# Kernel tuning notes

Measured on AMD Instinct MI355X. Metric: run time of the kernel, lower is better.

## Reference

```python
import math
import jax, jax.numpy as jnp
import numpy as np

N, C, H, W, G = 32, 128, 56, 56, 32
SHIFT = 1  # fixed value for random.randint(-1, 1) chosen at module init


def _unfold_h(x):
    # F.unfold(x, (3,1), dilation=(2,1), padding=(2,0)) -> (n, c, 3, h, w)
    p = jnp.pad(x, ((0, 0), (0, 0), (2, 2), (0, 0)))
    return jnp.stack([p[:, :, 0:H], p[:, :, 2:H + 2], p[:, :, 4:H + 4]], axis=2)


def _unfold_w(x):
    # F.unfold(x, (1,3), dilation=(1,2), padding=(0,2)) -> (n, c, 3, h, w)
    p = jnp.pad(x, ((0, 0), (0, 0), (0, 0), (2, 2)))
    return jnp.stack([p[:, :, :, 0:W], p[:, :, :, 2:W + 2], p[:, :, :, 4:W + 4]], axis=2)


def setup_inputs() -> dict:
    key = jax.random.key(0)
    k1, k2, k3, k4 = jax.random.split(key, 4)
    x = jax.random.normal(k1, (N, C, H, W), dtype=jnp.float32)
    p2w = jax.random.normal(k2, (1, C, 3, H, W), dtype=jnp.float32) * 0.02
    p5w = jax.random.normal(k3, (1, C, 1, 1), dtype=jnp.float32) * 0.02
    conv_w = jax.random.normal(k4, (C // G, C), dtype=jnp.float32) * 0.02  # 1x1 conv, no bias
    return {"x": x, "p2w": p2w, "p5w": p5w, "conv_w": conv_w}


def reference(x, p2w, p5w, conv_w):
    n = x.shape[0]
    t1 = _unfold_h(x)                      # (n, c, 3, h, w)
    t2 = p2w * t1                          # (n, c, 3, h, w)
    t3 = _unfold_w(x)                      # (n, c, 3, h, w)
    t4 = jnp.roll(x, SHIFT, axis=2)        # roll along height
    t5 = p5w * t4
    t6 = t4 + x
    t2f = t2.reshape(n, C * 3, H * W)
    t6f = t6.reshape(n, C, H * W)
    # bmm: (n, c*3, hw) x (n, hw, c) -> (n, c*3, c)
    t7 = jnp.einsum('nkp,ncp->nkc', t2f, t6f) / math.sqrt(H * W)
    # 1x1 conv: (c//g, c) applied pointwise
    t8 = jnp.einsum('oc,nchw->nohw', conv_w, t5)            # (n, c//g, h, w)
    t9 = (t8[:, None] * x.reshape(n, G, C // G, H, W)).reshape(n, C, H, W)
    t3f = t3.reshape(n, C * 3, H * W)
    # bmm: (n, c, c*3) x (n, c*3, hw) -> (n, c, hw)
    t10 = (jnp.einsum('nkc,nkp->ncp', t7, t3f) / math.sqrt(C * 3)).reshape(n, C, H, W)
    return t9 + t10
```

## Files before the change

### kernel.cpp

```cpp
#include <hip/hip_runtime.h>

#define NB 32
#define CCH 128
#define HH 56
#define WWD 56
#define HWP (HH*WWD)
#define K3C (3*CCH)
#define SPLITK 8

typedef _Float16 half8 __attribute__((ext_vector_type(8)));
typedef float floatx4 __attribute__((ext_vector_type(4)));

__global__ __launch_bounds__(256) void cvtp2w_kernel(const float* __restrict__ src,
                                                     _Float16* __restrict__ dst) {
    const int row = blockIdx.x;
    const int j = row >> 7;
    const int c = row & 127;
    const float* s = src + ((size_t)c * 3 + j) * HWP;
    _Float16* d = dst + (size_t)row * HWP;
    for (int base = threadIdx.x * 8; base < HWP; base += 2048) {
        const float4 a = *(const float4*)(s + base);
        const float4 b = *(const float4*)(s + base + 4);
        half8 v;
        v[0] = (_Float16)a.x; v[1] = (_Float16)a.y; v[2] = (_Float16)a.z; v[3] = (_Float16)a.w;
        v[4] = (_Float16)b.x; v[5] = (_Float16)b.y; v[6] = (_Float16)b.z; v[7] = (_Float16)b.w;
        *(half8*)(d + base) = v;
    }
}

__global__ __launch_bounds__(256) void cvt_xt_kernel(const float* __restrict__ x,
                                                     _Float16* __restrict__ xh,
                                                     _Float16* __restrict__ xT) {
    __shared__ _Float16 t[64 * 72];
    const int bid = blockIdx.x;
    const int r8  = bid & 7;
    const int g   = bid >> 3;
    const int n   = r8 + 8 * (g / 98);
    const int rem = g % 98;
    const int c0  = (rem / 49) * 64;
    const int p0  = (rem % 49) * 64;
    const int tid = threadIdx.x;
    const int r   = tid >> 2;
    const int seg = (tid & 3) * 16;

    const float* src = x + ((size_t)n * CCH + c0 + r) * HWP + p0 + seg;
    const float4 a0 = *(const float4*)(src);
    const float4 a1 = *(const float4*)(src + 4);
    const float4 a2 = *(const float4*)(src + 8);
    const float4 a3 = *(const float4*)(src + 12);
    half8 v0, v1;
    v0[0] = (_Float16)a0.x; v0[1] = (_Float16)a0.y; v0[2] = (_Float16)a0.z; v0[3] = (_Float16)a0.w;
    v0[4] = (_Float16)a1.x; v0[5] = (_Float16)a1.y; v0[6] = (_Float16)a1.z; v0[7] = (_Float16)a1.w;
    v1[0] = (_Float16)a2.x; v1[1] = (_Float16)a2.y; v1[2] = (_Float16)a2.z; v1[3] = (_Float16)a2.w;
    v1[4] = (_Float16)a3.x; v1[5] = (_Float16)a3.y; v1[6] = (_Float16)a3.z; v1[7] = (_Float16)a3.w;

    _Float16* dxh = xh + ((size_t)n * CCH + c0 + r) * HWP + p0 + seg;
    *(half8*)(dxh)     = v0;
    *(half8*)(dxh + 8) = v1;
    *(half8*)(&t[r * 72 + seg])     = v0;
    *(half8*)(&t[r * 72 + seg + 8]) = v1;
    __syncthreads();
    _Float16* dst = xT + ((size_t)n * HWP + p0 + r) * CCH + c0 + seg;
    half8 w0, w1;
#pragma unroll
    for (int i = 0; i < 8; ++i) w0[i] = t[(seg + i) * 72 + r];
#pragma unroll
    for (int i = 0; i < 8; ++i) w1[i] = t[(seg + 8 + i) * 72 + r];
    *(half8*)(dst) = w0;
    *(half8*)(dst + 8) = w1;
}

__global__ __launch_bounds__(64) void t8_kernel(const _Float16* __restrict__ xh,
                                                const float* __restrict__ conv_w,
                                                const float* __restrict__ p5w,
                                                float* __restrict__ t8) {
    const int bid = blockIdx.x;
    const int r8  = bid & 7;
    const int g   = bid >> 3;
    const int n   = r8 + 8 * (g / 49);
    const int p   = (g % 49) * 64 + threadIdx.x;
    const int proll = (p >= WWD) ? (p - WWD) : (p + (HH - 1) * WWD);
    const _Float16* xb = xh + (size_t)n * CCH * HWP + proll;
    float a0 = 0.f, a1 = 0.f, a2 = 0.f, a3 = 0.f;
#pragma unroll 4
    for (int c = 0; c < CCH; ++c) {
        const float xp = (float)xb[(size_t)c * HWP] * p5w[c];
        a0 += conv_w[c] * xp;
        a1 += conv_w[CCH + c] * xp;
        a2 += conv_w[2 * CCH + c] * xp;
        a3 += conv_w[3 * CCH + c] * xp;
    }
    float* dst = t8 + (size_t)n * 4 * HWP + p;
    dst[0] = a0; dst[HWP] = a1; dst[2 * HWP] = a2; dst[3 * HWP] = a3;
}

__global__ __launch_bounds__(256) void gemm1_kernel(const _Float16* __restrict__ xh,
                                                    const _Float16* __restrict__ p2wh,
                                                    _Float16* __restrict__ part) {
    __shared__ _Float16 As[128 * 72];
    __shared__ _Float16 Bs[128 * 72];

    const int bid   = blockIdx.x;
    const int r8    = bid & 7;
    const int g     = bid >> 3;
    const int n     = r8 + 8 * (g / 24);
    const int inner = g % 24;
    const int jb    = inner % 3;
    const int m0    = jb * 128;
    const int s     = inner / 3;
    const int i0    = (s * 49) >> 3;
    const int i1    = ((s + 1) * 49) >> 3;

    const int tid = threadIdx.x;
    const int r   = tid >> 1;
    const int c0  = (tid & 1) * 32;

    const int ashift = 112 * (jb - 1);
    const _Float16* xa = xh + ((size_t)n * CCH + r) * HWP;
    const _Float16* pw = p2wh + (size_t)(m0 + r) * HWP;

    const int wave = tid >> 6;
    const int lane = tid & 63;
    const int l15  = lane & 15;
    const int quad = lane >> 4;
    const int wm   = (wave >> 1) * 64;
    const int wn   = (wave & 1) * 64;

    floatx4 acc[4][4];
#pragma unroll
    for (int a = 0; a < 4; ++a)
#pragma unroll
        for (int b = 0; b < 4; ++b) acc[a][b] = (floatx4){0.f,0.f,0.f,0.f};

    half8 xv[4], wv[4], uv[4], vv[4];

    {
        const int p0 = i0 * 64;
#pragma unroll
        for (int seg = 0; seg < 4; ++seg) {
            const int col  = c0 + seg * 8;
            const int pA   = p0 + col;
            const int srcp = pA + ashift;
            if (srcp >= 0 && srcp < HWP) {
                xv[seg] = *(const half8*)(xa + srcp);
                wv[seg] = *(const half8*)(pw + pA);
            } else {
#pragma unroll
                for (int i = 0; i < 8; ++i) { xv[seg][i] = (_Float16)0.f; wv[seg][i] = (_Float16)0.f; }
            }
            const int proll = (pA >= WWD) ? (pA - WWD) : (pA + (HH - 1) * WWD);
            uv[seg] = *(const half8*)(xa + pA);
            vv[seg] = *(const half8*)(xa + proll);
        }
    }

    for (int it = i0; it < i1; ++it) {
#pragma unroll
        for (int seg = 0; seg < 4; ++seg) {
            const int col = c0 + seg * 8;
            *(half8*)(&As[r * 72 + col]) = xv[seg] * wv[seg];
            *(half8*)(&Bs[r * 72 + col]) = uv[seg] + vv[seg];
        }
        __syncthreads();
        if (it + 1 < i1) {
            const int p0 = (it + 1) * 64;
#pragma unroll
            for (int seg = 0; seg < 4; ++seg) {
                const int col  = c0 + seg * 8;
                const int pA   = p0 + col;
                const int srcp = pA + ashift;
                if (srcp >= 0 && srcp < HWP) {
                    xv[seg] = *(const half8*)(xa + srcp);
                    wv[seg] = *(const half8*)(pw + pA);
                } else {
#pragma unroll
                    for (int i = 0; i < 8; ++i) { xv[seg][i] = (_Float16)0.f; wv[seg][i] = (_Float16)0.f; }
                }
                const int proll = (pA >= WWD) ? (pA - WWD) : (pA + (HH - 1) * WWD);
                uv[seg] = *(const half8*)(xa + pA);
                vv[seg] = *(const half8*)(xa + proll);
            }
        }
#pragma unroll
        for (int ks = 0; ks < 2; ++ks) {
            const int ko = ks * 32 + quad * 8;
            half8 af[4], bf[4];
#pragma unroll
            for (int mi = 0; mi < 4; ++mi) af[mi] = *(half8*)(&As[(wm + mi * 16 + l15) * 72 + ko]);
#pragma unroll
            for (int ni = 0; ni < 4; ++ni) bf[ni] = *(half8*)(&Bs[(wn + ni * 16 + l15) * 72 + ko]);
#pragma unroll
            for (int mi = 0; mi < 4; ++mi)
#pragma unroll
                for (int ni = 0; ni < 4; ++ni)
                    acc[mi][ni] = __builtin_amdgcn_mfma_f32_16x16x32_f16(af[mi], bf[ni], acc[mi][ni], 0, 0, 0);
        }
        __syncthreads();
    }

    _Float16* pbase = part + (size_t)(s * NB + n) * K3C * CCH;
#pragma unroll
    for (int mi = 0; mi < 4; ++mi)
#pragma unroll
        for (int ni = 0; ni < 4; ++ni) {
            const int kr = m0 + wm + mi * 16 + quad * 4;
            const int cc = wn + ni * 16 + l15;
#pragma unroll
            for (int r2 = 0; r2 < 4; ++r2)
                pbase[(size_t)(kr + r2) * CCH + cc] = (_Float16)acc[mi][ni][r2];
        }
}

__global__ __launch_bounds__(256) void reduce_kernel(const _Float16* __restrict__ part,
                                                     _Float16* __restrict__ t7T) {
    __shared__ _Float16 tile[16][130];
    const int n  = blockIdx.y;
    const int k0 = blockIdx.x * 16;
    const int t  = threadIdx.x;
    const int c2 = t & 127;
    const int kh = t >> 7;
#pragma unroll
    for (int kk = 0; kk < 8; ++kk) {
        const int k = kh * 8 + kk;
        float sum = 0.f;
#pragma unroll
        for (int sp = 0; sp < SPLITK; ++sp)
            sum += (float)part[(((size_t)sp * NB + n) * K3C + k0 + k) * CCH + c2];
        tile[k][c2] = (_Float16)(sum * (1.0f / 56.0f));
    }
    __syncthreads();
    const int kt = t & 15;
    const int c0 = t >> 4;
#pragma unroll
    for (int cc = 0; cc < 8; ++cc) {
        const int cw = c0 * 8 + cc;
        t7T[((size_t)n * CCH + cw) * K3C + k0 + kt] = tile[kt][cw];
    }
}

__global__ __launch_bounds__(256) void gemm2_kernel(const _Float16* __restrict__ xh,
                                                    const _Float16* __restrict__ xT,
                                                    const _Float16* __restrict__ t7T,
                                                    const float* __restrict__ t8,
                                                    float* __restrict__ out) {
    __shared__ _Float16 As[128 * 72];
    __shared__ _Float16 Bs[64 * 72];

    const int bid = blockIdx.x;
    const int r8  = bid & 7;
    const int g   = bid >> 3;
    const int n   = r8 + 8 * (g / 49);
    const int pt0 = (g % 49) * 64;
    const int tid = threadIdx.x;

    const int ar = tid >> 1;
    const int ac = (tid & 1) * 32;
    const _Float16* asrc = t7T + ((size_t)n * CCH + ar) * K3C;

    const int rb   = tid >> 2;
    const int bseg = (tid & 3) * 16;
    const int pB   = pt0 + rb;
    const int hb   = pB / WWD;
    const int wb   = pB - hb * WWD;
    const _Float16* xTn = xT + (size_t)n * HWP * CCH;

    const int wave = tid >> 6;
    const int lane = tid & 63;
    const int l15  = lane & 15;
    const int quad = lane >> 4;
    const int wm   = (wave >> 1) * 64;
    const int wn   = (wave & 1) * 32;

    floatx4 acc[4][2];
#pragma unroll
    for (int a = 0; a < 4; ++a)
#pragma unroll
        for (int b = 0; b < 2; ++b) acc[a][b] = (floatx4){0.f,0.f,0.f,0.f};

    half8 av[4], bv0, bv1;

    {
#pragma unroll
        for (int seg = 0; seg < 4; ++seg)
            av[seg] = *(const half8*)(asrc + ac + seg * 8);
        const int wsrc = wb - 2;
        if (wsrc >= 0) {
            const _Float16* srcB = xTn + ((size_t)hb * WWD + wsrc) * CCH + bseg;
            bv0 = *(const half8*)(srcB);
            bv1 = *(const half8*)(srcB + 8);
        } else {
#pragma unroll
            for (int i = 0; i < 8; ++i) { bv0[i] = (_Float16)0.f; bv1[i] = (_Float16)0.f; }
        }
    }

#pragma unroll
    for (int k0 = 0; k0 < K3C; k0 += 64) {
#pragma unroll
        for (int seg = 0; seg < 4; ++seg)
            *(half8*)(&As[ar * 72 + ac + seg * 8]) = av[seg];
        *(half8*)(&Bs[rb * 72 + bseg])     = bv0;
        *(half8*)(&Bs[rb * 72 + bseg + 8]) = bv1;
        __syncthreads();
        if (k0 + 64 < K3C) {
            const int kn  = k0 + 64;
            const int jn  = kn >> 7;
            const int c0k = kn & 127;
#pragma unroll
            for (int seg = 0; seg < 4; ++seg)
                av[seg] = *(const half8*)(asrc + kn + ac + seg * 8);
            const int wsrc = wb + 2 * jn - 2;
            if (wsrc >= 0 && wsrc < WWD) {
                const _Float16* srcB = xTn + ((size_t)hb * WWD + wsrc) * CCH + c0k + bseg;
                bv0 = *(const half8*)(srcB);
                bv1 = *(const half8*)(srcB + 8);
            } else {
#pragma unroll
                for (int i = 0; i < 8; ++i) { bv0[i] = (_Float16)0.f; bv1[i] = (_Float16)0.f; }
            }
        }
#pragma unroll
        for (int ks = 0; ks < 2; ++ks) {
            const int ko = ks * 32 + quad * 8;
            half8 af[4], bf[2];
#pragma unroll
            for (int mi = 0; mi < 4; ++mi) af[mi] = *(half8*)(&As[(wm + mi * 16 + l15) * 72 + ko]);
#pragma unroll
            for (int ni = 0; ni < 2; ++ni) bf[ni] = *(half8*)(&Bs[(wn + ni * 16 + l15) * 72 + ko]);
#pragma unroll
            for (int mi = 0; mi < 4; ++mi)
#pragma unroll
                for (int ni = 0; ni < 2; ++ni)
                    acc[mi][ni] = __builtin_amdgcn_mfma_f32_16x16x32_f16(af[mi], bf[ni], acc[mi][ni], 0, 0, 0);
        }
        __syncthreads();
    }

    const float sc = 0.05103103630798288f;
#pragma unroll
    for (int mi = 0; mi < 4; ++mi)
#pragma unroll
        for (int ni = 0; ni < 2; ++ni) {
            const int ccb = wm + mi * 16 + quad * 4;
            const int pp  = pt0 + wn + ni * 16 + l15;
#pragma unroll
            for (int r2 = 0; r2 < 4; ++r2) {
                const int c2 = ccb + r2;
                const size_t oidx = ((size_t)n * CCH + c2) * HWP + pp;
                const float t9 = t8[((size_t)n * 4 + (c2 & 3)) * HWP + pp] * (float)xh[oidx];
                out[oidx] = acc[mi][ni][r2] * sc + t9;
            }
        }
}

extern "C" void kernel_launch(void* const* d_in, const int* in_sizes, int n_in,
                              void* d_out, int out_size, void* d_ws, size_t ws_size,
                              hipStream_t stream) {
    const float* x      = (const float*)d_in[0];
    const float* p2w    = (const float*)d_in[1];
    const float* p5w    = (const float*)d_in[2];
    const float* conv_w = (const float*)d_in[3];
    float* out = (float*)d_out;

    char* ws = (char*)d_ws;
    _Float16* xh   = (_Float16*)ws;
    _Float16* p2wh = (_Float16*)(ws + 25690112);
    float*    t8f  = (float*)   (ws + 25690112 + 2408448);
    _Float16* t7T  = (_Float16*)(ws + 25690112 + 2408448 + 1605632);
    _Float16* xT   = (_Float16*)(ws + 25690112 + 2408448 + 1605632 + 3145728);
    _Float16* part = (_Float16*)out;

    cvtp2w_kernel<<<dim3(K3C), dim3(256), 0, stream>>>(p2w, p2wh);
    cvt_xt_kernel<<<dim3(3136), dim3(256), 0, stream>>>(x, xh, xT);
    t8_kernel<<<dim3(1568), dim3(64), 0, stream>>>(xh, conv_w, p5w, t8f);
    gemm1_kernel<<<dim3(768), dim3(256), 0, stream>>>(xh, p2wh, part);
    reduce_kernel<<<dim3(24, NB), dim3(256), 0, stream>>>(part, t7T);
    gemm2_kernel<<<dim3(1568), dim3(256), 0, stream>>>(xh, xT, t7T, t8f, out);
}
```

Measured before the change: 205.6 us.

## Coalesce global loads in gemm1/gemm2 and rewrite t8 over transposed x

The t8 kernel now reads the channel-last xT copy through a shared-memory tile using 256 threads. It also folds p5w into conv_w in shared memory, which replaces the strided per-channel reads across HWP. The gemm1 and gemm2 tile loaders remap threads so that 8 consecutive threads cover a 64-element row in 16-byte chunks. This gives wider coalesced global transactions than the previous 2-4 threads per row. The arithmetic is unchanged, but the new t8 adds LDS traffic and a barrier.

New measurement: 180.7 us. -12.1%, faster.

```diff
diff --git a/kernel.cpp b/kernel.cpp
--- a/kernel.cpp
+++ b/kernel.cpp
@@ -70,28 +70,44 @@
     *(half8*)(dst + 8) = w1;
 }
 
-__global__ __launch_bounds__(64) void t8_kernel(const _Float16* __restrict__ xh,
-                                                const float* __restrict__ conv_w,
-                                                const float* __restrict__ p5w,
-                                                float* __restrict__ t8) {
+__global__ __launch_bounds__(256) void t8_kernel(const _Float16* __restrict__ xT,
+                                                 const float* __restrict__ conv_w,
+                                                 const float* __restrict__ p5w,
+                                                 float* __restrict__ t8) {
+    __shared__ _Float16 tile[64 * 136];
+    __shared__ float wf[4 * 128];
     const int bid = blockIdx.x;
     const int r8  = bid & 7;
     const int g   = bid >> 3;
     const int n   = r8 + 8 * (g / 49);
-    const int p   = (g % 49) * 64 + threadIdx.x;
-    const int proll = (p >= WWD) ? (p - WWD) : (p + (HH - 1) * WWD);
-    const _Float16* xb = xh + (size_t)n * CCH * HWP + proll;
-    float a0 = 0.f, a1 = 0.f, a2 = 0.f, a3 = 0.f;
-#pragma unroll 4
-    for (int c = 0; c < CCH; ++c) {
-        const float xp = (float)xb[(size_t)c * HWP] * p5w[c];
-        a0 += conv_w[c] * xp;
-        a1 += conv_w[CCH + c] * xp;
-        a2 += conv_w[2 * CCH + c] * xp;
-        a3 += conv_w[3 * CCH + c] * xp;
-    }
-    float* dst = t8 + (size_t)n * 4 * HWP + p;
-    dst[0] = a0; dst[HWP] = a1; dst[2 * HWP] = a2; dst[3 * HWP] = a3;
+    const int p0  = (g % 49) * 64;
+    const int tid = threadIdx.x;
+
+    wf[tid]       = conv_w[tid] * p5w[tid & 127];
+    wf[tid + 256] = conv_w[tid + 256] * p5w[tid & 127];
+
+    const int coff = (tid & 15) * 8;
+    const _Float16* xTn = xT + (size_t)n * HWP * CCH;
+#pragma unroll
+    for (int q = 0; q < 4; ++q) {
+        const int row = q * 16 + (tid >> 4);
+        const int p   = p0 + row;
+        const int srcrow = (p >= WWD) ? (p - WWD) : (p + (HH - 1) * WWD);
+        *(half8*)(&tile[row * 136 + coff]) = *(const half8*)(xTn + (size_t)srcrow * CCH + coff);
+    }
+    __syncthreads();
+
+    const int o  = tid >> 6;
+    const int pl = tid & 63;
+    const float* wrow = wf + o * 128;
+    float a = 0.f;
+#pragma unroll
+    for (int cs = 0; cs < 16; ++cs) {
+        const half8 v = *(const half8*)(&tile[pl * 136 + cs * 8]);
+#pragma unroll
+        for (int i = 0; i < 8; ++i) a += wrow[cs * 8 + i] * (float)v[i];
+    }
+    t8[((size_t)n * 4 + o) * HWP + p0 + pl] = a;
 }
 
 __global__ __launch_bounds__(256) void gemm1_kernel(const _Float16* __restrict__ xh,
@@ -111,13 +127,13 @@
     const int i0    = (s * 49) >> 3;
     const int i1    = ((s + 1) * 49) >> 3;
 
-    const int tid = threadIdx.x;
-    const int r   = tid >> 1;
-    const int c0  = (tid & 1) * 32;
+    const int tid  = threadIdx.x;
+    const int lrow = tid >> 3;
+    const int lcol = (tid & 7) * 8;
 
     const int ashift = 112 * (jb - 1);
-    const _Float16* xa = xh + ((size_t)n * CCH + r) * HWP;
-    const _Float16* pw = p2wh + (size_t)(m0 + r) * HWP;
+    const _Float16* xh_n = xh + (size_t)n * CCH * HWP;
+    const _Float16* pw_m = p2wh + (size_t)m0 * HWP;
 
     const int wave = tid >> 6;
     const int lane = tid & 63;
@@ -136,49 +152,45 @@
 
     {
         const int p0 = i0 * 64;
-#pragma unroll
-        for (int seg = 0; seg < 4; ++seg) {
-            const int col  = c0 + seg * 8;
-            const int pA   = p0 + col;
-            const int srcp = pA + ashift;
-            if (srcp >= 0 && srcp < HWP) {
-                xv[seg] = *(const half8*)(xa + srcp);
-                wv[seg] = *(const half8*)(pw + pA);
-            } else {
-#pragma unroll
-                for (int i = 0; i < 8; ++i) { xv[seg][i] = (_Float16)0.f; wv[seg][i] = (_Float16)0.f; }
-            }
-            const int proll = (pA >= WWD) ? (pA - WWD) : (pA + (HH - 1) * WWD);
-            uv[seg] = *(const half8*)(xa + pA);
-            vv[seg] = *(const half8*)(xa + proll);
+        const int pA = p0 + lcol;
+        const int srcp  = pA + ashift;
+        const int proll = (pA >= WWD) ? (pA - WWD) : (pA + (HH - 1) * WWD);
+        const bool ok = (srcp >= 0 && srcp < HWP);
+#pragma unroll
+        for (int sg = 0; sg < 4; ++sg) {
+            const int row = sg * 32 + lrow;
+            const _Float16* xaS = xh_n + (size_t)row * HWP;
+            if (ok) xv[sg] = *(const half8*)(xaS + srcp);
+            else { half8 z; for (int i = 0; i < 8; ++i) z[i] = (_Float16)0.f; xv[sg] = z; }
+            wv[sg] = *(const half8*)(pw_m + (size_t)row * HWP + pA);
+            uv[sg] = *(const half8*)(xaS + pA);
+            vv[sg] = *(const half8*)(xaS + proll);
         }
     }
 
     for (int it = i0; it < i1; ++it) {
 #pragma unroll
-        for (int seg = 0; seg < 4; ++seg) {
-            const int col = c0 + seg * 8;
-            *(half8*)(&As[r * 72 + col]) = xv[seg] * wv[seg];
-            *(half8*)(&Bs[r * 72 + col]) = uv[seg] + vv[seg];
+        for (int sg = 0; sg < 4; ++sg) {
+            const int row = sg * 32 + lrow;
+            *(half8*)(&As[row * 72 + lcol]) = xv[sg] * wv[sg];
+            *(half8*)(&Bs[row * 72 + lcol]) = uv[sg] + vv[sg];
         }
         __syncthreads();
         if (it + 1 < i1) {
             const int p0 = (it + 1) * 64;
-#pragma unroll
-            for (int seg = 0; seg < 4; ++seg) {
-                const int col  = c0 + seg * 8;
-                const int pA   = p0 + col;
-                const int srcp = pA + ashift;
-                if (srcp >= 0 && srcp < HWP) {
-                    xv[seg] = *(const half8*)(xa + srcp);
-                    wv[seg] = *(const half8*)(pw + pA);
-                } else {
-#pragma unroll
-                    for (int i = 0; i < 8; ++i) { xv[seg][i] = (_Float16)0.f; wv[seg][i] = (_Float16)0.f; }
-                }
-                const int proll = (pA >= WWD) ? (pA - WWD) : (pA + (HH - 1) * WWD);
-                uv[seg] = *(const half8*)(xa + pA);
-                vv[seg] = *(const half8*)(xa + proll);
+            const int pA = p0 + lcol;
+            const int srcp  = pA + ashift;
+            const int proll = (pA >= WWD) ? (pA - WWD) : (pA + (HH - 1) * WWD);
+            const bool ok = (srcp >= 0 && srcp < HWP);
+#pragma unroll
+            for (int sg = 0; sg < 4; ++sg) {
+                const int row = sg * 32 + lrow;
+                const _Float16* xaS = xh_n + (size_t)row * HWP;
+                if (ok) xv[sg] = *(const half8*)(xaS + srcp);
+                else { half8 z; for (int i = 0; i < 8; ++i) z[i] = (_Float16)0.f; xv[sg] = z; }
+                wv[sg] = *(const half8*)(pw_m + (size_t)row * HWP + pA);
+                uv[sg] = *(const half8*)(xaS + pA);
+                vv[sg] = *(const half8*)(xaS + proll);
             }
         }
 #pragma unroll
@@ -253,16 +265,19 @@
     const int pt0 = (g % 49) * 64;
     const int tid = threadIdx.x;
 
-    const int ar = tid >> 1;
-    const int ac = (tid & 1) * 32;
-    const _Float16* asrc = t7T + ((size_t)n * CCH + ar) * K3C;
-
-    const int rb   = tid >> 2;
-    const int bseg = (tid & 3) * 16;
-    const int pB   = pt0 + rb;
-    const int hb   = pB / WWD;
-    const int wb   = pB - hb * WWD;
+    const int lrow = tid >> 3;
+    const int lcol = (tid & 7) * 8;
+
+    const _Float16* t7n = t7T + (size_t)n * CCH * K3C;
     const _Float16* xTn = xT + (size_t)n * HWP * CCH;
+
+    int hbArr[2], wbArr[2];
+#pragma unroll
+    for (int sg = 0; sg < 2; ++sg) {
+        const int prow = pt0 + sg * 32 + lrow;
+        hbArr[sg] = prow / WWD;
+        wbArr[sg] = prow - hbArr[sg] * WWD;
+    }
 
     const int wave = tid >> 6;
     const int lane = tid & 63;
@@ -277,46 +292,47 @@
 #pragma unroll
         for (int b = 0; b < 2; ++b) acc[a][b] = (floatx4){0.f,0.f,0.f,0.f};
 
-    half8 av[4], bv0, bv1;
+    half8 av[4], bv[2];
 
     {
 #pragma unroll
-        for (int seg = 0; seg < 4; ++seg)
-            av[seg] = *(const half8*)(asrc + ac + seg * 8);
-        const int wsrc = wb - 2;
-        if (wsrc >= 0) {
-            const _Float16* srcB = xTn + ((size_t)hb * WWD + wsrc) * CCH + bseg;
-            bv0 = *(const half8*)(srcB);
-            bv1 = *(const half8*)(srcB + 8);
-        } else {
-#pragma unroll
-            for (int i = 0; i < 8; ++i) { bv0[i] = (_Float16)0.f; bv1[i] = (_Float16)0.f; }
+        for (int sg = 0; sg < 4; ++sg)
+            av[sg] = *(const half8*)(t7n + (size_t)(sg * 32 + lrow) * K3C + lcol);
+#pragma unroll
+        for (int sg = 0; sg < 2; ++sg) {
+            const int wsrc = wbArr[sg] - 2;
+            if (wsrc >= 0) {
+                bv[sg] = *(const half8*)(xTn + ((size_t)hbArr[sg] * WWD + wsrc) * CCH + lcol);
+            } else {
+                half8 z; for (int i = 0; i < 8; ++i) z[i] = (_Float16)0.f; bv[sg] = z;
+            }
         }
     }
 
 #pragma unroll
     for (int k0 = 0; k0 < K3C; k0 += 64) {
 #pragma unroll
-        for (int seg = 0; seg < 4; ++seg)
-            *(half8*)(&As[ar * 72 + ac + seg * 8]) = av[seg];
-        *(half8*)(&Bs[rb * 72 + bseg])     = bv0;
-        *(half8*)(&Bs[rb * 72 + bseg + 8]) = bv1;
+        for (int sg = 0; sg < 4; ++sg)
+            *(half8*)(&As[(sg * 32 + lrow) * 72 + lcol]) = av[sg];
+#pragma unroll
+        for (int sg = 0; sg < 2; ++sg)
+            *(half8*)(&Bs[(sg * 32 + lrow) * 72 + lcol]) = bv[sg];
         __syncthreads();
         if (k0 + 64 < K3C) {
             const int kn  = k0 + 64;
             const int jn  = kn >> 7;
             const int c0k = kn & 127;
 #pragma unroll
-            for (int seg = 0; seg < 4; ++seg)
-                av[seg] = *(const half8*)(asrc + kn + ac + seg * 8);
-            const int wsrc = wb + 2 * jn - 2;
-            if (wsrc >= 0 && wsrc < WWD) {
-                const _Float16* srcB = xTn + ((size_t)hb * WWD + wsrc) * CCH + c0k + bseg;
-                bv0 = *(const half8*)(srcB);
-                bv1 = *(const half8*)(srcB + 8);
-            } else {
-#pragma unroll
-                for (int i = 0; i < 8; ++i) { bv0[i] = (_Float16)0.f; bv1[i] = (_Float16)0.f; }
+            for (int sg = 0; sg < 4; ++sg)
+                av[sg] = *(const half8*)(t7n + (size_t)(sg * 32 + lrow) * K3C + kn + lcol);
+#pragma unroll
+            for (int sg = 0; sg < 2; ++sg) {
+                const int wsrc = wbArr[sg] + 2 * jn - 2;
+                if (wsrc >= 0 && wsrc < WWD) {
+                    bv[sg] = *(const half8*)(xTn + ((size_t)hbArr[sg] * WWD + wsrc) * CCH + c0k + lcol);
+                } else {
+                    half8 z; for (int i = 0; i < 8; ++i) z[i] = (_Float16)0.f; bv[sg] = z;
+                }
             }
         }
 #pragma unroll
@@ -372,7 +388,7 @@
 
     cvtp2w_kernel<<<dim3(K3C), dim3(256), 0, stream>>>(p2w, p2wh);
     cvt_xt_kernel<<<dim3(3136), dim3(256), 0, stream>>>(x, xh, xT);
-    t8_kernel<<<dim3(1568), dim3(64), 0, stream>>>(xh, conv_w, p5w, t8f);
+    t8_kernel<<<dim3(1568), dim3(256), 0, stream>>>(xT, conv_w, p5w, t8f);
     gemm1_kernel<<<dim3(768), dim3(256), 0, stream>>>(xh, p2wh, part);
     reduce_kernel<<<dim3(24, NB), dim3(256), 0, stream>>>(part, t7T);
     gemm2_kernel<<<dim3(1568), dim3(256), 0, stream>>>(xh, xT, t7T, t8f, out);
```
